# Optimization experiments

Measured on AMD Instinct MI355X. Metric: run time of the kernel, lower is better.

## Reference

```python
import jax, jax.numpy as jnp
import numpy as np
from jax import lax


def _lstm(x, h0, c0, w_ih, w_hh, b_ih, b_hh):
    """PyTorch-convention LSTM (gate order i,f,g,o). x: [B,T,D] -> ys [B,T,H], hT, cT."""
    xg = jnp.einsum('btd,gd->btg', x, w_ih) + b_ih + b_hh  # input projection hoisted out of scan

    def step(carry, xt):
        h, c = carry
        g = xt + h @ w_hh.T
        i, f, gg, o = jnp.split(g, 4, axis=-1)
        c = jax.nn.sigmoid(f) * c + jax.nn.sigmoid(i) * jnp.tanh(gg)
        h = jax.nn.sigmoid(o) * jnp.tanh(c)
        return (h, c), h

    (hT, cT), ys = lax.scan(step, (h0, c0), jnp.swapaxes(xg, 0, 1))
    return jnp.swapaxes(ys, 0, 1), hT, cT


def setup_inputs() -> dict:
    B, T_ENC, T_DEC = 256, 256, 256
    E, H, ME = 128, 512, 16
    NT = 30000
    G = 4 * H
    ks = iter(jax.random.split(jax.random.key(0), 64))

    def nrm(shape, s=0.05):
        return jax.random.normal(next(ks), shape, jnp.float32) * s

    enc_in = E + E + 2 * ME  # t_emb + a_emb + meta = 288
    dec_in = E + E + 2 * ME  # t_emb + meta + prev_a_emb = 288

    def lstm_params(din):
        return nrm((G, din)), nrm((G, H)), nrm((G,)), nrm((G,))

    bif_w_ih, bif_w_hh, bif_b_ih, bif_b_hh = lstm_params(enc_in)
    bib_w_ih, bib_w_hh, bib_b_ih, bib_b_hh = lstm_params(enc_in)
    enc_w_ih, enc_w_hh, enc_b_ih, enc_b_hh = lstm_params(2 * H)
    dec_w_ih, dec_w_hh, dec_b_ih, dec_b_hh = lstm_params(dec_in)

    inp = dict(
        enc_q=jax.random.randint(next(ks), (B, T_ENC), 0, NT + 2),
        enc_a=jax.random.randint(next(ks), (B, T_ENC), 0, 2),
        enc_pos=jax.random.randint(next(ks), (B, T_ENC), 0, 22),
        enc_fmt=jax.random.randint(next(ks), (B, T_ENC), 0, 7),
        dec_q=jax.random.randint(next(ks), (B, T_DEC), 0, NT + 2),
        dec_a=jax.random.randint(next(ks), (B, T_DEC), 0, 2),
        dec_pos=jax.random.randint(next(ks), (B, T_DEC), 0, 22),
        dec_fmt=jax.random.randint(next(ks), (B, T_DEC), 0, 7),
        enc_last_a=jax.random.randint(next(ks), (B,), 0, 2),
        t_emb_w=nrm((NT + 2, E)).at[0].set(0.0),  # padding_idx=0
        a_emb_w=nrm((2, E)),
        pos_emb_w=nrm((22, ME)).at[0].set(0.0),
        fmt_emb_w=nrm((7, ME)).at[0].set(0.0),
        bif_w_ih=bif_w_ih, bif_w_hh=bif_w_hh, bif_b_ih=bif_b_ih, bif_b_hh=bif_b_hh,
        bib_w_ih=bib_w_ih, bib_w_hh=bib_w_hh, bib_b_ih=bib_b_ih, bib_b_hh=bib_b_hh,
        enc_w_ih=enc_w_ih, enc_w_hh=enc_w_hh, enc_b_ih=enc_b_ih, enc_b_hh=enc_b_hh,
        dec_w_ih=dec_w_ih, dec_w_hh=dec_w_hh, dec_b_ih=dec_b_ih, dec_b_hh=dec_b_hh,
        pred_w1=nrm((H, E + 2 * ME + H)), pred_b1=nrm((H,)),
        pred_w2=nrm((1, H)), pred_b2=nrm((1,)),
    )
    return inp


def reference(enc_q, enc_a, enc_pos, enc_fmt, dec_q, dec_a, dec_pos, dec_fmt, enc_last_a,
              t_emb_w, a_emb_w, pos_emb_w, fmt_emb_w,
              bif_w_ih, bif_w_hh, bif_b_ih, bif_b_hh,
              bib_w_ih, bib_w_hh, bib_b_ih, bib_b_hh,
              enc_w_ih, enc_w_hh, enc_b_ih, enc_b_hh,
              dec_w_ih, dec_w_hh, dec_b_ih, dec_b_hh,
              pred_w1, pred_b1, pred_w2, pred_b2):
    B = enc_q.shape[0]
    H = bif_w_hh.shape[1]
    h0 = jnp.zeros((B, H), jnp.float32)

    # ----- encode (full-length sequences; dropout = identity in eval) -----
    enc_x = jnp.concatenate([t_emb_w[enc_q], a_emb_w[enc_a],
                             pos_emb_w[enc_pos], fmt_emb_w[enc_fmt]], axis=-1)
    fwd_out, _, _ = _lstm(enc_x, h0, h0, bif_w_ih, bif_w_hh, bif_b_ih, bif_b_hh)
    bwd_out, _, _ = _lstm(enc_x[:, ::-1], h0, h0, bib_w_ih, bib_w_hh, bib_b_ih, bib_b_hh)
    bi_out = jnp.concatenate([fwd_out, bwd_out[:, ::-1]], axis=-1)  # [B,T,2H]
    _, hN, cN = _lstm(bi_out, h0, h0, enc_w_ih, enc_w_hh, enc_b_ih, enc_b_hh)

    # ----- decode (teacher forcing: prev answers = shifted dec_a) -----
    prev_a = jnp.concatenate([enc_last_a[:, None], dec_a[:, :-1]], axis=1)
    dec_t = t_emb_w[dec_q]                                            # [B,T,E]
    dec_m = jnp.concatenate([pos_emb_w[dec_pos], fmt_emb_w[dec_fmt]], axis=-1)
    dec_x = jnp.concatenate([dec_t, dec_m, a_emb_w[prev_a]], axis=-1)  # cat order as in decode()
    dec_out, _, _ = _lstm(dec_x, hN, cN, dec_w_ih, dec_w_hh, dec_b_ih, dec_b_hh)

    pred_in = jnp.concatenate([dec_t, dec_m, dec_out], axis=-1)       # [B,T,E+2*ME+H]
    hidden = jnp.tanh(pred_in @ pred_w1.T + pred_b1)
    logits = hidden @ pred_w2.T + pred_b2                              # [B,T,1]
    return jax.nn.sigmoid(logits[..., 0])                              # [B,T]
```

## Files before the change

### kernel.cpp

```cpp
#include <hip/hip_runtime.h>


using u16 = unsigned short;
using u32 = unsigned int;
using u64 = unsigned long long;
typedef float f32x4 __attribute__((ext_vector_type(4)));
typedef __bf16 bf16x8 __attribute__((ext_vector_type(8)));

__device__ __forceinline__ u16 f2bf(float f) {
  u32 u = __float_as_uint(f);
  u = (u + 0x7FFFu + ((u >> 16) & 1u)) >> 16;
  return (u16)u;
}
__device__ __forceinline__ float bf2f(u16 h) { return __uint_as_float(((u32)h) << 16); }
__device__ __forceinline__ float sigm(float x) { return 1.f / (1.f + __expf(-x)); }
__device__ __forceinline__ float tnh(float x) {
  float a = fabsf(x), e = __expf(-2.f * a);
  float t = (1.f - e) / (1.f + e);
  return x < 0.f ? -t : t;
}
__device__ __forceinline__ u64 ldA_u64(const u16* p) {
  return __hip_atomic_load((const u64*)p, __ATOMIC_RELAXED, __HIP_MEMORY_SCOPE_AGENT);
}
__device__ __forceinline__ void stA_u16(u16* p, u16 v) {
  __hip_atomic_store(p, v, __ATOMIC_RELAXED, __HIP_MEMORY_SCOPE_AGENT);
}
__device__ __forceinline__ void gload_lds16(const u16* g, u16* l) {
  __builtin_amdgcn_global_load_lds(
      (const __attribute__((address_space(1))) unsigned int*)g,
      (__attribute__((address_space(3))) unsigned int*)l, 16, 0, 0);
}

static const long SLOT_BI = 256L * 1024;
static const long SLOT_DO = 256L * 512;
static const long SLOT_XG = 256L * 2048;

template <int ACT, int KSTEPS>
__global__ __launch_bounds__(256) void gemm_tile_k(
    const u16* __restrict__ A1, long lda1, const u16* __restrict__ A2, long lda2, int ksplit,
    const u16* __restrict__ W, long ldw, const float* __restrict__ bias,
    u16* __restrict__ C, long ldc) {
  __shared__ u16 sA[4096];
  __shared__ u16 sB[4096];
  const int tid = threadIdx.x;
  const int w = tid >> 6, lane = tid & 63;
  const int lr = lane & 15, lg = lane >> 4;
  const long mbase = (long)blockIdx.y * 128;
  const long nbase = (long)blockIdx.x * 128;
  const int wm = (w >> 1) * 64, wn = (w & 1) * 64;
  const int s_r = lane >> 2, s_q = lane & 3;
  f32x4 acc[4][4] = {};
#pragma unroll 1
  for (int ks = 0; ks < KSTEPS; ks++) {
    const int kk = ks * 32;
    const u16* Asrc;
    long alda;
    int kofs;
    if (kk < ksplit) { Asrc = A1; alda = lda1; kofs = kk; }
    else             { Asrc = A2; alda = lda2; kofs = kk - ksplit; }
#pragma unroll
    for (int j = 0; j < 2; j++) {
      const int c = w * 2 + j;
      const long row = c * 16 + s_r;
      gload_lds16(Asrc + (mbase + row) * alda + kofs + s_q * 8, sA + c * 512);
      gload_lds16(W + (nbase + row) * ldw + kk + s_q * 8, sB + c * 512);
    }
    __syncthreads();
    bf16x8 a[4], b[4];
#pragma unroll
    for (int f = 0; f < 4; f++) {
      a[f] = *reinterpret_cast<const bf16x8*>(sA + (wm + f * 16 + lr) * 32 + lg * 8);
      b[f] = *reinterpret_cast<const bf16x8*>(sB + (wn + f * 16 + lr) * 32 + lg * 8);
    }
#pragma unroll
    for (int fm = 0; fm < 4; fm++)
#pragma unroll
      for (int fn = 0; fn < 4; fn++)
        acc[fm][fn] = __builtin_amdgcn_mfma_f32_16x16x32_bf16(a[fm], b[fn], acc[fm][fn], 0, 0, 0);
    __syncthreads();
  }
#pragma unroll
  for (int fm = 0; fm < 4; fm++)
#pragma unroll
    for (int fn = 0; fn < 4; fn++)
#pragma unroll
      for (int r = 0; r < 4; r++) {
        const long row = mbase + wm + fm * 16 + lg * 4 + r;
        const long col = nbase + wn + fn * 16 + lr;
        float v = acc[fm][fn][r] + bias[col];
        if (ACT == 1) v = tnh(v);
        C[row * ldc + col] = f2bf(v);
      }
}

struct SeqP {
  const u16 *xgA, *xgB;
  const u16 *whA, *whB;
  float *cA, *cB;
  u16 *histA;
  u16 *h0, *h1;
  u32 *cnt;
  int k, CH;
};

template <int MODE>
__global__ __launch_bounds__(512, 2) void lstm_seq_k(SeqP p) {
  const int tid = threadIdx.x;
  const int w = tid >> 6, lane = tid & 63, lr = lane & 15, lg = lane >> 4;
  const int hct = w & 3, kh = w >> 2;
  int dir, rt, kb;
  if (MODE == 0) { dir = blockIdx.x >> 7; rt = (blockIdx.x >> 3) & 15; kb = blockIdx.x & 7; }
  else           { dir = 0;               rt = blockIdx.x >> 3;        kb = blockIdx.x & 7; }
  const u16* xg = (MODE == 0 && dir) ? p.xgB : p.xgA;
  const u16* wh = (MODE == 0 && dir) ? p.whB : p.whA;
  float* cbuf   = (MODE == 0 && dir) ? p.cB  : p.cA;
  const int rbase = rt * 16;
  const int hc0 = kb * 64 + hct * 16;
  const int kofs = kh * 256;
  u32* cnt = p.cnt + (long)((MODE == 0) ? (dir * 16 + rt) : rt) * 32;

  bf16x8 W[4][8];
#pragma unroll
  for (int g = 0; g < 4; g++)
#pragma unroll
    for (int ki = 0; ki < 8; ki++)
      W[g][ki] = *reinterpret_cast<const bf16x8*>(
          wh + (long)(g * 512 + hc0 + lr) * 512 + kofs + ki * 32 + lg * 8);

  const bool zero_init = (MODE <= 1) && (p.k == 0);
  float creg[4];
#pragma unroll
  for (int r = 0; r < 4; r++) {
    creg[r] = 0.f;
    if (kh == 0 && !zero_init)
      creg[r] = cbuf[(long)(rbase + lg * 4 + r) * 512 + hc0 + lr];
  }

  __shared__ f32x4 lacc[4][4][64];

  for (int ts = 0; ts < p.CH; ts++) {
    const int S = p.k * p.CH + ts;
    const u16* hp;
    u16* ho;
    long hstride;
    int slot;
    bool first;
    if (MODE == 0) {
      const int t = dir == 0 ? S : 255 - S;
      slot = dir == 0 ? ts : p.CH - 1 - ts;
      hstride = 1024;
      const int tp = dir == 0 ? t - 1 : t + 1;
      hp = p.histA + (long)tp * SLOT_BI + dir * 512;
      ho = p.histA + (long)t * SLOT_BI + dir * 512;
      first = (S == 0);
    } else if (MODE == 1) {
      slot = ts; hstride = 512;
      hp = (S & 1) ? p.h1 : p.h0;
      ho = (S & 1) ? p.h0 : p.h1;
      first = (S == 0);
    } else {
      slot = ts; hstride = 512;
      hp = (S == 0) ? p.h0 : p.histA + (long)((S - 1) & (p.CH - 1)) * SLOT_DO;
      ho = p.histA + (long)(S & (p.CH - 1)) * SLOT_DO;
      first = false;
    }

    u16 xv[4][4];
    if (kh == 0) {
      const long xbase = (long)slot * SLOT_XG;
      const int colh = hc0 + lr;
#pragma unroll
      for (int r = 0; r < 4; r++) {
        const long xr = xbase + (long)(rbase + lg * 4 + r) * 2048 + colh;
#pragma unroll
        for (int g = 0; g < 4; g++) xv[r][g] = xg[xr + g * 512];
      }
    }

    f32x4 acc[4] = {};
    if (!first) {
      union AU { u64 q[2]; bf16x8 v; } au[8];
      const u16* abase = hp + (long)(rbase + lr) * hstride + kofs;
#pragma unroll
      for (int ki = 0; ki < 8; ki++) {
        au[ki].q[0] = ldA_u64(abase + ki * 32 + lg * 8);
        au[ki].q[1] = ldA_u64(abase + ki * 32 + lg * 8 + 4);
      }
#pragma unroll
      for (int ki = 0; ki < 8; ki++) {
#pragma unroll
        for (int g = 0; g < 4; g++)
          acc[g] = __builtin_amdgcn_mfma_f32_16x16x32_bf16(au[ki].v, W[g][ki], acc[g], 0, 0, 0);
      }
    }
    if (kh == 1) {
#pragma unroll
      for (int g = 0; g < 4; g++) lacc[hct][g][lane] = acc[g];
    }
    __syncthreads();
    if (kh == 0) {
#pragma unroll
      for (int g = 0; g < 4; g++) acc[g] += lacc[hct][g][lane];
#pragma unroll
      for (int r = 0; r < 4; r++) {
        const long row = rbase + lg * 4 + r;
        const int colh = hc0 + lr;
        float gi = acc[0][r] + bf2f(xv[r][0]);
        float gf = acc[1][r] + bf2f(xv[r][1]);
        float gg = acc[2][r] + bf2f(xv[r][2]);
        float go = acc[3][r] + bf2f(xv[r][3]);
        float cn = sigm(gf) * creg[r] + sigm(gi) * tnh(gg);
        creg[r] = cn;
        stA_u16(&ho[row * hstride + colh], f2bf(sigm(go) * tnh(cn)));
      }
    }
    __syncthreads();
    if (tid == 0) {
      __hip_atomic_fetch_add(cnt, 1u, __ATOMIC_RELAXED, __HIP_MEMORY_SCOPE_AGENT);
      if (ts != p.CH - 1) {
        const u32 tgt = 8u * (u32)(S + 1);
        while (__hip_atomic_load(cnt, __ATOMIC_RELAXED, __HIP_MEMORY_SCOPE_AGENT) < tgt)
          __builtin_amdgcn_s_sleep(1);
      }
    }
    __syncthreads();
  }
  if (kh == 0) {
#pragma unroll
    for (int r = 0; r < 4; r++)
      cbuf[(long)(rbase + lg * 4 + r) * 512 + hc0 + lr] = creg[r];
  }
}

struct WcvP {
  const float* s[9]; u16* d[9]; long n[9];
  const float *ba[4], *bb[4]; float* bd[4];
};
__global__ __launch_bounds__(256) void initw_k(WcvP w) {
  const long g0 = (long)blockIdx.x * 256 + threadIdx.x;
  const long gs = (long)gridDim.x * 256;
  for (int seg = 0; seg < 9; seg++)
    for (long i = g0; i < w.n[seg]; i += gs) w.d[seg][i] = f2bf(w.s[seg][i]);
  for (int seg = 0; seg < 4; seg++)
    for (long i = g0; i < 2048; i += gs) w.bd[seg][i] = w.ba[seg][i] + w.bb[seg][i];
}

__global__ __launch_bounds__(256) void embed_enc_k(
    const int* __restrict__ q, const int* __restrict__ a, const int* __restrict__ pos,
    const int* __restrict__ fmt, const float* __restrict__ tw, const float* __restrict__ aw,
    const float* __restrict__ pw, const float* __restrict__ fw, u16* __restrict__ out) {
  for (long row = blockIdx.x; row < 65536; row += gridDim.x) {
    const int t = (int)(row >> 8), b = (int)(row & 255);
    const long src = (long)b * 256 + t;
    const int iq = q[src], ia = a[src], ip = pos[src], ifm = fmt[src];
    for (int col = threadIdx.x; col < 288; col += 256) {
      float v;
      if (col < 128)      v = tw[(long)iq * 128 + col];
      else if (col < 256) v = aw[(long)ia * 128 + (col - 128)];
      else if (col < 272) v = pw[(long)ip * 16 + (col - 256)];
      else                v = fw[(long)ifm * 16 + (col - 272)];
      out[row * 288 + col] = f2bf(v);
    }
  }
}

__global__ __launch_bounds__(256) void embed_dec_k(
    const int* __restrict__ q, const int* __restrict__ a, const int* __restrict__ pos,
    const int* __restrict__ fmt, const int* __restrict__ last_a,
    const float* __restrict__ tw, const float* __restrict__ aw,
    const float* __restrict__ pw, const float* __restrict__ fw, u16* __restrict__ out) {
  for (long row = blockIdx.x; row < 65536; row += gridDim.x) {
    const int t = (int)(row >> 8), b = (int)(row & 255);
    const long src = (long)b * 256 + t;
    const int iq = q[src], ip = pos[src], ifm = fmt[src];
    const int pa = (t == 0) ? last_a[b] : a[src - 1];
    for (int col = threadIdx.x; col < 288; col += 256) {
      float v;
      if (col < 128)      v = tw[(long)iq * 128 + col];
      else if (col < 144) v = pw[(long)ip * 16 + (col - 128)];
      else if (col < 160) v = fw[(long)ifm * 16 + (col - 144)];
      else                v = aw[(long)pa * 128 + (col - 160)];
      out[row * 288 + col] = f2bf(v);
    }
  }
}

__global__ __launch_bounds__(256) void pred_out_k(
    const u16* __restrict__ hidden, const float* __restrict__ w2,
    const float* __restrict__ b2, float* __restrict__ out, int t0) {
  const long r = (long)blockIdx.x * 4 + (threadIdx.x >> 6);
  const int lane = threadIdx.x & 63;
  const u16* hp = hidden + r * 512 + lane * 8;
  const float* wp = w2 + lane * 8;
  float s = 0.f;
#pragma unroll
  for (int j = 0; j < 8; j++) s += bf2f(hp[j]) * wp[j];
  for (int off = 32; off > 0; off >>= 1) s += __shfl_down(s, off);
  if (lane == 0) out[(r & 255) * 256 + t0 + (r >> 8)] = sigm(s + b2[0]);
}

__global__ __launch_bounds__(256) void zero_k(u32* __restrict__ p, int n) {
  int i = blockIdx.x * 256 + threadIdx.x;
  if (i < n) p[i] = 0;
}

extern "C" void kernel_launch(void* const* d_in, const int* in_sizes, int n_in,
                              void* d_out, int out_size, void* d_ws, size_t ws_size,
                              hipStream_t stream) {
  const int* enc_q     = (const int*)d_in[0];
  const int* enc_a     = (const int*)d_in[1];
  const int* enc_pos   = (const int*)d_in[2];
  const int* enc_fmt   = (const int*)d_in[3];
  const int* dec_q     = (const int*)d_in[4];
  const int* dec_a     = (const int*)d_in[5];
  const int* dec_pos   = (const int*)d_in[6];
  const int* dec_fmt   = (const int*)d_in[7];
  const int* enc_last  = (const int*)d_in[8];
  const float* t_emb   = (const float*)d_in[9];
  const float* a_emb   = (const float*)d_in[10];
  const float* pos_emb = (const float*)d_in[11];
  const float* fmt_emb = (const float*)d_in[12];
  const float* bif_w_ih = (const float*)d_in[13];
  const float* bif_w_hh = (const float*)d_in[14];
  const float* bif_b_ih = (const float*)d_in[15];
  const float* bif_b_hh = (const float*)d_in[16];
  const float* bib_w_ih = (const float*)d_in[17];
  const float* bib_w_hh = (const float*)d_in[18];
  const float* bib_b_ih = (const float*)d_in[19];
  const float* bib_b_hh = (const float*)d_in[20];
  const float* enc_w_ih = (const float*)d_in[21];
  const float* enc_w_hh = (const float*)d_in[22];
  const float* enc_b_ih = (const float*)d_in[23];
  const float* enc_b_hh = (const float*)d_in[24];
  const float* dec_w_ih = (const float*)d_in[25];
  const float* dec_w_hh = (const float*)d_in[26];
  const float* dec_b_ih = (const float*)d_in[27];
  const float* dec_b_hh = (const float*)d_in[28];
  const float* pred_w1 = (const float*)d_in[29];
  const float* pred_b1 = (const float*)d_in[30];
  const float* pred_w2 = (const float*)d_in[31];
  const float* pred_b2 = (const float*)d_in[32];
  (void)in_sizes; (void)n_in; (void)out_size;

  char* base = (char*)d_ws;
  size_t off = 0;
  auto alloc = [&](size_t bytes) -> char* {
    char* p = base + off;
    off = (off + bytes + 255) & ~(size_t)255;
    return p;
  };

  u16* wb_bif_ih = (u16*)alloc(2048L * 288 * 2);
  u16* wb_bib_ih = (u16*)alloc(2048L * 288 * 2);
  u16* wb_enc_ih = (u16*)alloc(2048L * 1024 * 2);
  u16* wb_dec_ih = (u16*)alloc(2048L * 288 * 2);
  u16* wb_bif_hh = (u16*)alloc(2048L * 512 * 2);
  u16* wb_bib_hh = (u16*)alloc(2048L * 512 * 2);
  u16* wb_enc_hh = (u16*)alloc(2048L * 512 * 2);
  u16* wb_dec_hh = (u16*)alloc(2048L * 512 * 2);
  u16* wb_pred1  = (u16*)alloc(512L * 672 * 2);
  float* bias_bif = (float*)alloc(2048 * 4);
  float* bias_bib = (float*)alloc(2048 * 4);
  float* bias_enc = (float*)alloc(2048 * 4);
  float* bias_dec = (float*)alloc(2048 * 4);
  float* c_bif = (float*)alloc(256L * 512 * 4);
  float* c_bib = (float*)alloc(256L * 512 * 4);
  float* c_enc = (float*)alloc(256L * 512 * 4);
  u16* h_enc0 = (u16*)alloc(256L * 512 * 2);
  u16* h_enc1 = (u16*)alloc(256L * 512 * 2);
  u32* cnt = (u32*)alloc(64L * 32 * 4);

  u16* bi    = (u16*)alloc(65536L * 1024 * 2);
  u16* dec_x = (u16*)alloc(65536L * 288 * 2);
  u16* enc_x = (u16*)alloc(65536L * 288 * 2);

  int CH = 64;
  while (CH > 8 && off + 2ull * CH * 256 * 2048 * 2 > ws_size) CH >>= 1;
  u16* X1 = (u16*)alloc((size_t)CH * 256 * 2048 * 2);
  u16* X2 = (u16*)alloc((size_t)CH * 256 * 2048 * 2);
  u16* decout = enc_x;
  u16* hidden = enc_x + (long)CH * 256 * 512;
  const int NCH = 256 / CH;

  zero_k<<<8, 256, 0, stream>>>(cnt, 64 * 32);

  WcvP wc;
  wc.s[0] = bif_w_ih; wc.d[0] = wb_bif_ih; wc.n[0] = 2048L * 288;
  wc.s[1] = bib_w_ih; wc.d[1] = wb_bib_ih; wc.n[1] = 2048L * 288;
  wc.s[2] = enc_w_ih; wc.d[2] = wb_enc_ih; wc.n[2] = 2048L * 1024;
  wc.s[3] = dec_w_ih; wc.d[3] = wb_dec_ih; wc.n[3] = 2048L * 288;
  wc.s[4] = bif_w_hh; wc.d[4] = wb_bif_hh; wc.n[4] = 2048L * 512;
  wc.s[5] = bib_w_hh; wc.d[5] = wb_bib_hh; wc.n[5] = 2048L * 512;
  wc.s[6] = enc_w_hh; wc.d[6] = wb_enc_hh; wc.n[6] = 2048L * 512;
  wc.s[7] = dec_w_hh; wc.d[7] = wb_dec_hh; wc.n[7] = 2048L * 512;
  wc.s[8] = pred_w1;  wc.d[8] = wb_pred1;  wc.n[8] = 512L * 672;
  wc.ba[0] = bif_b_ih; wc.bb[0] = bif_b_hh; wc.bd[0] = bias_bif;
  wc.ba[1] = bib_b_ih; wc.bb[1] = bib_b_hh; wc.bd[1] = bias_bib;
  wc.ba[2] = enc_b_ih; wc.bb[2] = enc_b_hh; wc.bd[2] = bias_enc;
  wc.ba[3] = dec_b_ih; wc.bb[3] = dec_b_hh; wc.bd[3] = bias_dec;
  initw_k<<<1024, 256, 0, stream>>>(wc);

  embed_enc_k<<<2048, 256, 0, stream>>>(enc_q, enc_a, enc_pos, enc_fmt,
                                        t_emb, a_emb, pos_emb, fmt_emb, enc_x);
  embed_dec_k<<<2048, 256, 0, stream>>>(dec_q, dec_a, dec_pos, dec_fmt, enc_last,
                                        t_emb, a_emb, pos_emb, fmt_emb, dec_x);

  for (int k = 0; k < NCH; k++) {
    const int t0f = k * CH;
    const int t0b = 256 - (k + 1) * CH;
    gemm_tile_k<0, 9><<<dim3(16, CH * 2), 256, 0, stream>>>(
        enc_x + (long)t0f * 256 * 288, 288, enc_x, 288, 288,
        wb_bif_ih, 288, bias_bif, X1, 2048);
    gemm_tile_k<0, 9><<<dim3(16, CH * 2), 256, 0, stream>>>(
        enc_x + (long)t0b * 256 * 288, 288, enc_x, 288, 288,
        wb_bib_ih, 288, bias_bib, X2, 2048);
    SeqP sp{X1, X2, wb_bif_hh, wb_bib_hh, c_bif, c_bib,
            bi, nullptr, nullptr, cnt, k, CH};
    lstm_seq_k<0><<<dim3(256), dim3(512), 0, stream>>>(sp);
  }

  for (int k = 0; k < NCH; k++) {
    const int t0 = k * CH;
    gemm_tile_k<0, 32><<<dim3(16, CH * 2), 256, 0, stream>>>(
        bi + (long)t0 * SLOT_BI, 1024, bi, 1024, 1024,
        wb_enc_ih, 1024, bias_enc, X1, 2048);
    SeqP sp{X1, nullptr, wb_enc_hh, nullptr, c_enc, nullptr,
            nullptr, h_enc0, h_enc1, cnt + 32L * 32, k, CH};
    lstm_seq_k<1><<<dim3(128), dim3(512), 0, stream>>>(sp);
  }

  for (int k = 0; k < NCH; k++) {
    const int t0 = k * CH;
    gemm_tile_k<0, 9><<<dim3(16, CH * 2), 256, 0, stream>>>(
        dec_x + (long)t0 * 256 * 288, 288, dec_x, 288, 288,
        wb_dec_ih, 288, bias_dec, X1, 2048);
    SeqP sp{X1, nullptr, wb_dec_hh, nullptr, c_enc, nullptr,
            decout, h_enc0, nullptr, cnt + 48L * 32, k, CH};
    lstm_seq_k<2><<<dim3(128), dim3(512), 0, stream>>>(sp);
    gemm_tile_k<1, 21><<<dim3(4, CH * 2), 256, 0, stream>>>(
        dec_x + (long)t0 * 256 * 288, 288, decout, 512, 160,
        wb_pred1, 672, pred_b1, hidden, 512);
    pred_out_k<<<CH * 64, 256, 0, stream>>>(hidden, pred_w2, pred_b2, (float*)d_out, t0);
  }
}
```

Measured before the change: 6.471 ms.

## Interleave gate columns, merge bi-dir input GEMMs, enlarge chunks, batch prediction head

The input-projection GEMMs now write their outputs with the four gate columns interleaved, so each LSTM step thread fetches its i,f,g,o preactivations in a single 64-bit load instead of four scattered 16-bit loads. The forward and backward encoder projections are merged into one launch via a z-dimension, and the time chunk grows from 64 to 128 steps, which halves the number of sequential-kernel launches. The decoder writes its full hidden history into the bi buffer so the prediction head runs once over all timesteps after the loop rather than once per chunk. In exchange this needs a larger workspace, lets the chunk size fall back when memory is short, and reuses the bi buffer after the encoder has finished with it.

Result: faster. 6.239 ms (-3.6%).

```diff
diff --git a/kernel.cpp b/kernel.cpp
--- a/kernel.cpp
+++ b/kernel.cpp
@@ -35,18 +35,16 @@
 static const long SLOT_DO = 256L * 512;
 static const long SLOT_XG = 256L * 2048;
 
-template <int ACT, int KSTEPS>
-__global__ __launch_bounds__(256) void gemm_tile_k(
+template <int ACT, int KSTEPS, int PERM>
+__device__ __forceinline__ void gemm_body(
     const u16* __restrict__ A1, long lda1, const u16* __restrict__ A2, long lda2, int ksplit,
     const u16* __restrict__ W, long ldw, const float* __restrict__ bias,
-    u16* __restrict__ C, long ldc) {
-  __shared__ u16 sA[4096];
-  __shared__ u16 sB[4096];
+    u16* __restrict__ C, long ldc, int bx, int by, u16* sA, u16* sB) {
   const int tid = threadIdx.x;
   const int w = tid >> 6, lane = tid & 63;
   const int lr = lane & 15, lg = lane >> 4;
-  const long mbase = (long)blockIdx.y * 128;
-  const long nbase = (long)blockIdx.x * 128;
+  const long mbase = (long)by * 128;
+  const long nbase = (long)bx * 128;
   const int wm = (w >> 1) * 64, wn = (w & 1) * 64;
   const int s_r = lane >> 2, s_q = lane & 3;
   f32x4 acc[4][4] = {};
@@ -89,8 +87,36 @@
         const long col = nbase + wn + fn * 16 + lr;
         float v = acc[fm][fn][r] + bias[col];
         if (ACT == 1) v = tnh(v);
-        C[row * ldc + col] = f2bf(v);
+        const long cw = PERM ? (((col & 511) << 2) | (col >> 9)) : col;
+        C[row * ldc + cw] = f2bf(v);
       }
+}
+
+template <int ACT, int KSTEPS, int PERM>
+__global__ __launch_bounds__(256) void gemm_tile_k(
+    const u16* __restrict__ A1, long lda1, const u16* __restrict__ A2, long lda2, int ksplit,
+    const u16* __restrict__ W, long ldw, const float* __restrict__ bias,
+    u16* __restrict__ C, long ldc) {
+  __shared__ u16 sA[4096];
+  __shared__ u16 sB[4096];
+  gemm_body<ACT, KSTEPS, PERM>(A1, lda1, A2, lda2, ksplit, W, ldw, bias, C, ldc,
+                               blockIdx.x, blockIdx.y, sA, sB);
+}
+
+struct XGJob2 {
+  const u16 *Aa, *Ab, *Wa, *Wb;
+  const float *ba, *bb;
+  u16 *Xa, *Xb;
+};
+__global__ __launch_bounds__(256) void gemm_xg2_k(XGJob2 j) {
+  __shared__ u16 sA[4096];
+  __shared__ u16 sB[4096];
+  if (blockIdx.z == 0)
+    gemm_body<0, 9, 1>(j.Aa, 288, nullptr, 0, 1 << 30, j.Wa, 288, j.ba, j.Xa, 2048,
+                       blockIdx.x, blockIdx.y, sA, sB);
+  else
+    gemm_body<0, 9, 1>(j.Ab, 288, nullptr, 0, 1 << 30, j.Wb, 288, j.bb, j.Xb, 2048,
+                       blockIdx.x, blockIdx.y, sA, sB);
 }
 
 struct SeqP {
@@ -160,21 +186,19 @@
       first = (S == 0);
     } else {
       slot = ts; hstride = 512;
-      hp = (S == 0) ? p.h0 : p.histA + (long)((S - 1) & (p.CH - 1)) * SLOT_DO;
-      ho = p.histA + (long)(S & (p.CH - 1)) * SLOT_DO;
+      hp = (S == 0) ? p.h0 : p.histA + (long)(S - 1) * SLOT_DO;
+      ho = p.histA + (long)S * SLOT_DO;
       first = false;
     }
 
-    u16 xv[4][4];
+    u64 xq[4];
     if (kh == 0) {
-      const long xbase = (long)slot * SLOT_XG;
+      const long xb2 = (long)slot * SLOT_XG;
       const int colh = hc0 + lr;
 #pragma unroll
-      for (int r = 0; r < 4; r++) {
-        const long xr = xbase + (long)(rbase + lg * 4 + r) * 2048 + colh;
-#pragma unroll
-        for (int g = 0; g < 4; g++) xv[r][g] = xg[xr + g * 512];
-      }
+      for (int r = 0; r < 4; r++)
+        xq[r] = *reinterpret_cast<const u64*>(
+            xg + xb2 + (long)(rbase + lg * 4 + r) * 2048 + colh * 4);
     }
 
     f32x4 acc[4] = {};
@@ -205,10 +229,10 @@
       for (int r = 0; r < 4; r++) {
         const long row = rbase + lg * 4 + r;
         const int colh = hc0 + lr;
-        float gi = acc[0][r] + bf2f(xv[r][0]);
-        float gf = acc[1][r] + bf2f(xv[r][1]);
-        float gg = acc[2][r] + bf2f(xv[r][2]);
-        float go = acc[3][r] + bf2f(xv[r][3]);
+        float gi = acc[0][r] + bf2f((u16)(xq[r]));
+        float gf = acc[1][r] + bf2f((u16)(xq[r] >> 16));
+        float gg = acc[2][r] + bf2f((u16)(xq[r] >> 32));
+        float go = acc[3][r] + bf2f((u16)(xq[r] >> 48));
         float cn = sigm(gf) * creg[r] + sigm(gi) * tnh(gg);
         creg[r] = cn;
         stA_u16(&ho[row * hstride + colh], f2bf(sigm(go) * tnh(cn)));
@@ -287,7 +311,7 @@
 
 __global__ __launch_bounds__(256) void pred_out_k(
     const u16* __restrict__ hidden, const float* __restrict__ w2,
-    const float* __restrict__ b2, float* __restrict__ out, int t0) {
+    const float* __restrict__ b2, float* __restrict__ out) {
   const long r = (long)blockIdx.x * 4 + (threadIdx.x >> 6);
   const int lane = threadIdx.x & 63;
   const u16* hp = hidden + r * 512 + lane * 8;
@@ -296,7 +320,7 @@
 #pragma unroll
   for (int j = 0; j < 8; j++) s += bf2f(hp[j]) * wp[j];
   for (int off = 32; off > 0; off >>= 1) s += __shfl_down(s, off);
-  if (lane == 0) out[(r & 255) * 256 + t0 + (r >> 8)] = sigm(s + b2[0]);
+  if (lane == 0) out[(r & 255) * 256 + (r >> 8)] = sigm(s + b2[0]);
 }
 
 __global__ __launch_bounds__(256) void zero_k(u32* __restrict__ p, int n) {
@@ -374,12 +398,12 @@
   u16* dec_x = (u16*)alloc(65536L * 288 * 2);
   u16* enc_x = (u16*)alloc(65536L * 288 * 2);
 
-  int CH = 64;
+  int CH = 128;
   while (CH > 8 && off + 2ull * CH * 256 * 2048 * 2 > ws_size) CH >>= 1;
   u16* X1 = (u16*)alloc((size_t)CH * 256 * 2048 * 2);
   u16* X2 = (u16*)alloc((size_t)CH * 256 * 2048 * 2);
-  u16* decout = enc_x;
-  u16* hidden = enc_x + (long)CH * 256 * 512;
+  u16* decout = bi;
+  u16* hidden = bi + 65536L * 512;
   const int NCH = 256 / CH;
 
   zero_k<<<8, 256, 0, stream>>>(cnt, 64 * 32);
@@ -408,12 +432,9 @@
   for (int k = 0; k < NCH; k++) {
     const int t0f = k * CH;
     const int t0b = 256 - (k + 1) * CH;
-    gemm_tile_k<0, 9><<<dim3(16, CH * 2), 256, 0, stream>>>(
-        enc_x + (long)t0f * 256 * 288, 288, enc_x, 288, 288,
-        wb_bif_ih, 288, bias_bif, X1, 2048);
-    gemm_tile_k<0, 9><<<dim3(16, CH * 2), 256, 0, stream>>>(
-        enc_x + (long)t0b * 256 * 288, 288, enc_x, 288, 288,
-        wb_bib_ih, 288, bias_bib, X2, 2048);
+    XGJob2 j{enc_x + (long)t0f * 256 * 288, enc_x + (long)t0b * 256 * 288,
+             wb_bif_ih, wb_bib_ih, bias_bif, bias_bib, X1, X2};
+    gemm_xg2_k<<<dim3(16, CH * 2, 2), 256, 0, stream>>>(j);
     SeqP sp{X1, X2, wb_bif_hh, wb_bib_hh, c_bif, c_bib,
             bi, nullptr, nullptr, cnt, k, CH};
     lstm_seq_k<0><<<dim3(256), dim3(512), 0, stream>>>(sp);
@@ -421,7 +442,7 @@
 
   for (int k = 0; k < NCH; k++) {
     const int t0 = k * CH;
-    gemm_tile_k<0, 32><<<dim3(16, CH * 2), 256, 0, stream>>>(
+    gemm_tile_k<0, 32, 1><<<dim3(16, CH * 2), 256, 0, stream>>>(
         bi + (long)t0 * SLOT_BI, 1024, bi, 1024, 1024,
         wb_enc_ih, 1024, bias_enc, X1, 2048);
     SeqP sp{X1, nullptr, wb_enc_hh, nullptr, c_enc, nullptr,
@@ -431,15 +452,15 @@
 
   for (int k = 0; k < NCH; k++) {
     const int t0 = k * CH;
-    gemm_tile_k<0, 9><<<dim3(16, CH * 2), 256, 0, stream>>>(
+    gemm_tile_k<0, 9, 1><<<dim3(16, CH * 2), 256, 0, stream>>>(
         dec_x + (long)t0 * 256 * 288, 288, dec_x, 288, 288,
         wb_dec_ih, 288, bias_dec, X1, 2048);
     SeqP sp{X1, nullptr, wb_dec_hh, nullptr, c_enc, nullptr,
             decout, h_enc0, nullptr, cnt + 48L * 32, k, CH};
     lstm_seq_k<2><<<dim3(128), dim3(512), 0, stream>>>(sp);
-    gemm_tile_k<1, 21><<<dim3(4, CH * 2), 256, 0, stream>>>(
-        dec_x + (long)t0 * 256 * 288, 288, decout, 512, 160,
-        wb_pred1, 672, pred_b1, hidden, 512);
-    pred_out_k<<<CH * 64, 256, 0, stream>>>(hidden, pred_w2, pred_b2, (float*)d_out, t0);
-  }
-}
+  }
+
+  gemm_tile_k<1, 21, 0><<<dim3(4, 512), 256, 0, stream>>>(
+      dec_x, 288, decout, 512, 160, wb_pred1, 672, pred_b1, hidden, 512);
+  pred_out_k<<<16384, 256, 0, stream>>>(hidden, pred_w2, pred_b2, (float*)d_out);
+}
```
